# Performance work log

Hardware: AMD Instinct MI355X
Metric: run time of the kernel (lower is better)

## Reference

```python
import jax, jax.numpy as jnp
import numpy as np

H, W = 480, 640
FX, FY, CX, CY = 582.62, 582.69, 313.04, 238.44
B = 32

def _abc_const(ox, oy):
    # [3,H,W] back-projection grid: ((x+ox-cx)/fx, (y+oy-cy)/fy, 1)
    xs = (jnp.arange(W, dtype=jnp.float32) + ox - CX) / FX
    ys = (jnp.arange(H, dtype=jnp.float32) + oy - CY) / FY
    A = jnp.broadcast_to(xs[None, :], (H, W))
    Bc = jnp.broadcast_to(ys[:, None], (H, W))
    C = jnp.ones((H, W), jnp.float32)
    return jnp.stack([A, Bc, C], axis=0)

def _shift(x, mode):
    # matches elementwise_shift: zero-filled border
    if mode == 'left':
        return jnp.pad(x[..., 1:], ((0, 0), (0, 0), (0, 0), (0, 1)))
    if mode == 'right':
        return jnp.pad(x[..., :-1], ((0, 0), (0, 0), (0, 0), (1, 0)))
    if mode == 'up':
        return jnp.pad(x[..., 1:, :], ((0, 0), (0, 0), (0, 1), (0, 0)))
    return jnp.pad(x[..., :-1, :], ((0, 0), (0, 0), (1, 0), (0, 0)))  # down

def _safe_div(a, b):
    z = (b == 0)
    return jnp.where(z, 0.0, a / jnp.where(z, 1.0, b))

def setup_inputs() -> dict:
    key = jax.random.key(0)
    k1, k2 = jax.random.split(key)
    depth_input = jax.random.uniform(k1, (B, 1, H, W), dtype=jnp.float32)
    normal_input = jax.random.normal(k2, (B, 3, H, W), dtype=jnp.float32)
    return {"depth_input": depth_input, "normal_input": normal_input}

def reference(depth_input, normal_input):
    # ABC_sum: per-pixel dot of normal with mode-shifted XY1 grid -> [B,1,H,W]
    abc = lambda ox, oy: jnp.sum(_abc_const(ox, oy)[None] * normal_input,
                                 axis=1, keepdims=True)
    ABC_right = abc(1, 0)
    ABC_left = abc(-1, 0)
    ABC_up = abc(0, -1)
    ABC_down = abc(0, 1)
    z_i_left = _shift(depth_input, 'right')
    z_i_right = _shift(depth_input, 'left')
    z_i_up = _shift(depth_input, 'down')
    z_i_down = _shift(depth_input, 'up')
    z_o_right = _shift(_safe_div(ABC_left, ABC_right) * z_i_left, 'right')
    z_o_left = _shift(_safe_div(ABC_right, ABC_left) * z_i_right, 'left')
    z_o_down = _shift(_safe_div(ABC_up, ABC_down) * z_i_up, 'down')
    z_o_up = _shift(_safe_div(ABC_down, ABC_up) * z_i_down, 'up')
    return jnp.concatenate([z_o_up, z_o_down, z_o_left, z_o_right], axis=1)
```

## Files before the change

### kernel.cpp

```cpp
#include <hip/hip_runtime.h>

typedef float v4f __attribute__((ext_vector_type(4)));

namespace {
constexpr int H = 480, W = 640, B = 32;
constexpr int HW = H * W;
constexpr int W4 = W / 4;
constexpr int BLOCK = 256;
constexpr int NWG = B * H * W4 / BLOCK;
constexpr int PER_XCD = NWG / 8;
constexpr float CXf = 313.04f, CYf = 238.44f;
constexpr float RCPX = 1.0f / 582.62f;
constexpr float RCPY = 1.0f / 582.69f;
}

__device__ __forceinline__ float fmul_ieee(float a, float b) {
    float r; asm("v_mul_f32 %0, %1, %2" : "=v"(r) : "v"(a), "v"(b)); return r;
}
__device__ __forceinline__ float fadd_ieee(float a, float b) {
    float r; asm("v_add_f32 %0, %1, %2" : "=v"(r) : "v"(a), "v"(b)); return r;
}
__device__ __forceinline__ float abc_dot(float A, float Bv, float a0, float a1, float a2) {
    return fadd_ieee(fadd_ieee(fmul_ieee(A, a0), fmul_ieee(Bv, a1)), a2);
}
__device__ __forceinline__ float gx(int i) { return fmul_ieee((float)i - CXf, RCPX); }
__device__ __forceinline__ float gy(int i) { return fmul_ieee((float)i - CYf, RCPY); }

__device__ __forceinline__ float fast_ratio(float num, float den) {
    return num * __builtin_amdgcn_rcpf(den);
}

__device__ __forceinline__ void ld4(const float* p, float* a) {
    v4f v = *reinterpret_cast<const v4f*>(p);
    a[0] = v.x; a[1] = v.y; a[2] = v.z; a[3] = v.w;
}

__global__ __launch_bounds__(BLOCK) void znext_kernel(
    const float* __restrict__ depth,
    const float* __restrict__ normal,
    float* __restrict__ out)
{
    int bid = blockIdx.x;
    int wg = (bid & 7) * PER_XCD + (bid >> 3);
    int cid = wg * BLOCK + (int)threadIdx.x;
    int b = cid / (H * W4);
    int r = cid - b * (H * W4);
    int y = r / W4;
    int x0 = (r - y * W4) * 4;

    const float* d  = depth + (size_t)b * HW;
    const float* n0 = normal + (size_t)b * 3 * HW;
    const float* n1 = n0 + HW;
    const float* n2 = n1 + HW;

    int rowY = y * W;
    int rU  = min(y + 1, H - 1) * W;
    int rD  = max(y - 1, 0) * W;
    int rU2 = min(y + 2, H - 1) * W;
    int rD2 = max(y - 2, 0) * W;

    float nU[3][4], nD[3][4], nY[3][4];
    ld4(n0 + rU + x0, nU[0]); ld4(n1 + rU + x0, nU[1]); ld4(n2 + rU + x0, nU[2]);
    ld4(n0 + rD + x0, nD[0]); ld4(n1 + rD + x0, nD[1]); ld4(n2 + rD + x0, nD[2]);
    ld4(n0 + rowY + x0, nY[0]); ld4(n1 + rowY + x0, nY[1]); ld4(n2 + rowY + x0, nY[2]);
    float dU[4], dD[4], dY[4];
    ld4(d + rU2 + x0, dU); ld4(d + rD2 + x0, dD); ld4(d + rowY + x0, dY);

    int xm1 = max(x0 - 1, 0), xm2 = max(x0 - 2, 0);
    int xp4 = min(x0 + 4, W - 1), xp5 = min(x0 + 5, W - 1);
    float nL0 = n0[rowY + xm1], nL1 = n1[rowY + xm1], nL2 = n2[rowY + xm1];
    float nR0 = n0[rowY + xp4], nR1 = n1[rowY + xp4], nR2 = n2[rowY + xp4];
    float dm2 = d[rowY + xm2], dm1 = d[rowY + xm1];
    float dp4 = d[rowY + xp4], dp5 = d[rowY + xp5];

    float By  = gy(y);
    float BnU = gy(y + 2);
    float BnD = gy(y - 2);
    bool okU = (y < H - 2), okD = (y >= 2);

    float zu[4], zd[4], zl[4], zr[4];
#pragma unroll
    for (int j = 0; j < 4; ++j) {
        int x = x0 + j;
        float Ax = gx(x);
        {
            float num = abc_dot(Ax, BnU, nU[0][j], nU[1][j], nU[2][j]);
            float den = abc_dot(Ax, By,  nU[0][j], nU[1][j], nU[2][j]);
            zu[j] = (okU && den != 0.0f) ? fast_ratio(num, den) * dU[j] : 0.0f;
        }
        {
            float num = abc_dot(Ax, BnD, nD[0][j], nD[1][j], nD[2][j]);
            float den = abc_dot(Ax, By,  nD[0][j], nD[1][j], nD[2][j]);
            zd[j] = (okD && den != 0.0f) ? fast_ratio(num, den) * dD[j] : 0.0f;
        }
        {
            float a0 = (j < 3) ? nY[0][j + 1] : nR0;
            float a1 = (j < 3) ? nY[1][j + 1] : nR1;
            float a2 = (j < 3) ? nY[2][j + 1] : nR2;
            float dd = (j < 2) ? dY[j + 2] : ((j == 2) ? dp4 : dp5);
            float num = abc_dot(gx(x + 2), By, a0, a1, a2);
            float den = abc_dot(Ax,        By, a0, a1, a2);
            zl[j] = ((x < W - 2) && den != 0.0f) ? fast_ratio(num, den) * dd : 0.0f;
        }
        {
            float a0 = (j > 0) ? nY[0][j - 1] : nL0;
            float a1 = (j > 0) ? nY[1][j - 1] : nL1;
            float a2 = (j > 0) ? nY[2][j - 1] : nL2;
            float dd = (j >= 2) ? dY[j - 2] : ((j == 0) ? dm2 : dm1);
            float num = abc_dot(gx(x - 2), By, a0, a1, a2);
            float den = abc_dot(Ax,        By, a0, a1, a2);
            zr[j] = ((x >= 2) && den != 0.0f) ? fast_ratio(num, den) * dd : 0.0f;
        }
    }

    float* o = out + (size_t)b * 4 * HW + rowY + x0;
    v4f vu = { zu[0], zu[1], zu[2], zu[3] };
    v4f vd = { zd[0], zd[1], zd[2], zd[3] };
    v4f vl = { zl[0], zl[1], zl[2], zl[3] };
    v4f vr = { zr[0], zr[1], zr[2], zr[3] };
    __builtin_nontemporal_store(vu, reinterpret_cast<v4f*>(o));
    __builtin_nontemporal_store(vd, reinterpret_cast<v4f*>(o + HW));
    __builtin_nontemporal_store(vl, reinterpret_cast<v4f*>(o + 2 * HW));
    __builtin_nontemporal_store(vr, reinterpret_cast<v4f*>(o + 3 * HW));
}

extern "C" void kernel_launch(void* const* d_in, const int* in_sizes, int n_in,
                              void* d_out, int out_size, void* d_ws, size_t ws_size,
                              hipStream_t stream) {
    const float* depth  = (const float*)d_in[0];
    const float* normal = (const float*)d_in[1];
    float* out = (float*)d_out;
    znext_kernel<<<NWG, BLOCK, 0, stream>>>(depth, normal, out);
}
```

Baseline: 52.22 us.

## Compute two output rows per thread to reuse vertical neighbor loads

Each thread now handles two consecutive rows instead of one and halves the grid. Normal rows are loaded once and shared between the two rows' up/down stencils, so fewer redundant global loads are issued per output. The cost is higher register pressure and fewer threads, which may lower occupancy and latency hiding in a memory-bound kernel.

```diff
diff --git a/kernel.cpp b/kernel.cpp
--- a/kernel.cpp
+++ b/kernel.cpp
@@ -7,7 +7,7 @@
 constexpr int HW = H * W;
 constexpr int W4 = W / 4;
 constexpr int BLOCK = 256;
-constexpr int NWG = B * H * W4 / BLOCK;
+constexpr int NWG = B * (H / 2) * W4 / BLOCK;
 constexpr int PER_XCD = NWG / 8;
 constexpr float CXf = 313.04f, CYf = 238.44f;
 constexpr float RCPX = 1.0f / 582.62f;
@@ -35,49 +35,14 @@
     a[0] = v.x; a[1] = v.y; a[2] = v.z; a[3] = v.w;
 }
 
-__global__ __launch_bounds__(BLOCK) void znext_kernel(
-    const float* __restrict__ depth,
-    const float* __restrict__ normal,
-    float* __restrict__ out)
+__device__ __forceinline__ void compute_row(
+    int x0, float By, float BnU, float BnD, bool okU, bool okD,
+    const float nU[3][4], const float nD[3][4], const float nY[3][4],
+    float nL0, float nL1, float nL2, float nR0, float nR1, float nR2,
+    const float dU[4], const float dD[4], const float dY[4],
+    float dm2, float dm1, float dp4, float dp5,
+    v4f& vu, v4f& vd, v4f& vl, v4f& vr)
 {
-    int bid = blockIdx.x;
-    int wg = (bid & 7) * PER_XCD + (bid >> 3);
-    int cid = wg * BLOCK + (int)threadIdx.x;
-    int b = cid / (H * W4);
-    int r = cid - b * (H * W4);
-    int y = r / W4;
-    int x0 = (r - y * W4) * 4;
-
-    const float* d  = depth + (size_t)b * HW;
-    const float* n0 = normal + (size_t)b * 3 * HW;
-    const float* n1 = n0 + HW;
-    const float* n2 = n1 + HW;
-
-    int rowY = y * W;
-    int rU  = min(y + 1, H - 1) * W;
-    int rD  = max(y - 1, 0) * W;
-    int rU2 = min(y + 2, H - 1) * W;
-    int rD2 = max(y - 2, 0) * W;
-
-    float nU[3][4], nD[3][4], nY[3][4];
-    ld4(n0 + rU + x0, nU[0]); ld4(n1 + rU + x0, nU[1]); ld4(n2 + rU + x0, nU[2]);
-    ld4(n0 + rD + x0, nD[0]); ld4(n1 + rD + x0, nD[1]); ld4(n2 + rD + x0, nD[2]);
-    ld4(n0 + rowY + x0, nY[0]); ld4(n1 + rowY + x0, nY[1]); ld4(n2 + rowY + x0, nY[2]);
-    float dU[4], dD[4], dY[4];
-    ld4(d + rU2 + x0, dU); ld4(d + rD2 + x0, dD); ld4(d + rowY + x0, dY);
-
-    int xm1 = max(x0 - 1, 0), xm2 = max(x0 - 2, 0);
-    int xp4 = min(x0 + 4, W - 1), xp5 = min(x0 + 5, W - 1);
-    float nL0 = n0[rowY + xm1], nL1 = n1[rowY + xm1], nL2 = n2[rowY + xm1];
-    float nR0 = n0[rowY + xp4], nR1 = n1[rowY + xp4], nR2 = n2[rowY + xp4];
-    float dm2 = d[rowY + xm2], dm1 = d[rowY + xm1];
-    float dp4 = d[rowY + xp4], dp5 = d[rowY + xp5];
-
-    float By  = gy(y);
-    float BnU = gy(y + 2);
-    float BnD = gy(y - 2);
-    bool okU = (y < H - 2), okD = (y >= 2);
-
     float zu[4], zd[4], zl[4], zr[4];
 #pragma unroll
     for (int j = 0; j < 4; ++j) {
@@ -112,16 +77,83 @@
             zr[j] = ((x >= 2) && den != 0.0f) ? fast_ratio(num, den) * dd : 0.0f;
         }
     }
+    vu = v4f{ zu[0], zu[1], zu[2], zu[3] };
+    vd = v4f{ zd[0], zd[1], zd[2], zd[3] };
+    vl = v4f{ zl[0], zl[1], zl[2], zl[3] };
+    vr = v4f{ zr[0], zr[1], zr[2], zr[3] };
+}
 
-    float* o = out + (size_t)b * 4 * HW + rowY + x0;
-    v4f vu = { zu[0], zu[1], zu[2], zu[3] };
-    v4f vd = { zd[0], zd[1], zd[2], zd[3] };
-    v4f vl = { zl[0], zl[1], zl[2], zl[3] };
-    v4f vr = { zr[0], zr[1], zr[2], zr[3] };
-    __builtin_nontemporal_store(vu, reinterpret_cast<v4f*>(o));
-    __builtin_nontemporal_store(vd, reinterpret_cast<v4f*>(o + HW));
-    __builtin_nontemporal_store(vl, reinterpret_cast<v4f*>(o + 2 * HW));
-    __builtin_nontemporal_store(vr, reinterpret_cast<v4f*>(o + 3 * HW));
+__global__ __launch_bounds__(BLOCK) void znext_kernel(
+    const float* __restrict__ depth,
+    const float* __restrict__ normal,
+    float* __restrict__ out)
+{
+    int bid = blockIdx.x;
+    int wg = (bid & 7) * PER_XCD + (bid >> 3);
+    int cid = wg * BLOCK + (int)threadIdx.x;
+    constexpr int PERB = (H / 2) * W4;
+    int b = cid / PERB;
+    int r = cid - b * PERB;
+    int yh = r / W4;
+    int y0 = yh * 2;
+    int x0 = (r - yh * W4) * 4;
+
+    const float* d  = depth + (size_t)b * HW;
+    const float* n0 = normal + (size_t)b * 3 * HW;
+    const float* n1 = n0 + HW;
+    const float* n2 = n1 + HW;
+
+    int r0 = y0 * W;
+    int r1 = (y0 + 1) * W;
+    int rm1 = max(y0 - 1, 0) * W;
+    int r2 = min(y0 + 2, H - 1) * W;
+    int dm2r = max(y0 - 2, 0) * W;
+    int dp3r = min(y0 + 3, H - 1) * W;
+
+    float n_m1[3][4], n_0[3][4], n_1[3][4], n_2[3][4];
+    ld4(n0 + rm1 + x0, n_m1[0]); ld4(n1 + rm1 + x0, n_m1[1]); ld4(n2 + rm1 + x0, n_m1[2]);
+    ld4(n0 + r0  + x0, n_0[0]);  ld4(n1 + r0  + x0, n_0[1]);  ld4(n2 + r0  + x0, n_0[2]);
+    ld4(n0 + r1  + x0, n_1[0]);  ld4(n1 + r1  + x0, n_1[1]);  ld4(n2 + r1  + x0, n_1[2]);
+    ld4(n0 + r2  + x0, n_2[0]);  ld4(n1 + r2  + x0, n_2[1]);  ld4(n2 + r2  + x0, n_2[2]);
+
+    float d_m2[4], d_m1[4], d_0[4], d_1[4], d_p2[4], d_p3[4];
+    ld4(d + dm2r + x0, d_m2); ld4(d + rm1 + x0, d_m1); ld4(d + r0 + x0, d_0);
+    ld4(d + r1 + x0, d_1);    ld4(d + r2 + x0, d_p2);  ld4(d + dp3r + x0, d_p3);
+
+    int xm1 = max(x0 - 1, 0), xm2 = max(x0 - 2, 0);
+    int xp4 = min(x0 + 4, W - 1), xp5 = min(x0 + 5, W - 1);
+    float nL0a = n0[r0 + xm1], nL1a = n1[r0 + xm1], nL2a = n2[r0 + xm1];
+    float nR0a = n0[r0 + xp4], nR1a = n1[r0 + xp4], nR2a = n2[r0 + xp4];
+    float dm2a = d[r0 + xm2], dm1a = d[r0 + xm1], dp4a = d[r0 + xp4], dp5a = d[r0 + xp5];
+    float nL0b = n0[r1 + xm1], nL1b = n1[r1 + xm1], nL2b = n2[r1 + xm1];
+    float nR0b = n0[r1 + xp4], nR1b = n1[r1 + xp4], nR2b = n2[r1 + xp4];
+    float dm2b = d[r1 + xm2], dm1b = d[r1 + xm1], dp4b = d[r1 + xp4], dp5b = d[r1 + xp5];
+
+    v4f vu0, vd0, vl0, vr0;
+    compute_row(x0, gy(y0), gy(y0 + 2), gy(y0 - 2),
+                (y0 < H - 2), (y0 >= 2),
+                n_1, n_m1, n_0,
+                nL0a, nL1a, nL2a, nR0a, nR1a, nR2a,
+                d_p2, d_m2, d_0, dm2a, dm1a, dp4a, dp5a,
+                vu0, vd0, vl0, vr0);
+    v4f vu1, vd1, vl1, vr1;
+    compute_row(x0, gy(y0 + 1), gy(y0 + 3), gy(y0 - 1),
+                (y0 + 1 < H - 2), (y0 + 1 >= 2),
+                n_2, n_0, n_1,
+                nL0b, nL1b, nL2b, nR0b, nR1b, nR2b,
+                d_p3, d_m1, d_1, dm2b, dm1b, dp4b, dp5b,
+                vu1, vd1, vl1, vr1);
+
+    float* o = out + (size_t)b * 4 * HW + r0 + x0;
+    __builtin_nontemporal_store(vu0, reinterpret_cast<v4f*>(o));
+    __builtin_nontemporal_store(vd0, reinterpret_cast<v4f*>(o + HW));
+    __builtin_nontemporal_store(vl0, reinterpret_cast<v4f*>(o + 2 * HW));
+    __builtin_nontemporal_store(vr0, reinterpret_cast<v4f*>(o + 3 * HW));
+    float* o1 = o + W;
+    __builtin_nontemporal_store(vu1, reinterpret_cast<v4f*>(o1));
+    __builtin_nontemporal_store(vd1, reinterpret_cast<v4f*>(o1 + HW));
+    __builtin_nontemporal_store(vl1, reinterpret_cast<v4f*>(o1 + 2 * HW));
+    __builtin_nontemporal_store(vr1, reinterpret_cast<v4f*>(o1 + 3 * HW));
 }
 
 extern "C" void kernel_launch(void* const* d_in, const int* in_sizes, int n_in,
```

After: 53.52 us. 2.5% more time.
